# Performance work log

Measured on AMD Instinct MI355X. Metric: run time of the kernel, lower is better.

Reference implementation:

```python
import jax, jax.numpy as jnp
import numpy as np

B, I, H = 16384, 1024, 1024
W_SCALE = 0.03  # keep gate pre-activations in a sane range (mimics small init)


def setup_inputs() -> dict:
    key = jax.random.key(0)
    ks = jax.random.split(key, 7)
    return {
        "x": jax.random.normal(ks[0], (B, I), dtype=jnp.float32),
        "c": jax.random.normal(ks[1], (B, H), dtype=jnp.float32),
        "h": jax.random.normal(ks[2], (B, H), dtype=jnp.float32),
        # gate order along axis 0: f (forget), i (input), k (cell cand), o (output)
        "Wx": jax.random.normal(ks[3], (4, H, I), dtype=jnp.float32) * W_SCALE,
        "bx": jax.random.normal(ks[4], (4, H), dtype=jnp.float32) * W_SCALE,
        "Wh": jax.random.normal(ks[5], (4, H, H), dtype=jnp.float32) * W_SCALE,
        "bh": jax.random.normal(ks[6], (4, H), dtype=jnp.float32) * W_SCALE,
    }


def reference(x, c, h, Wx, bx, Wh, bh):
    # Fused equivalent of the 8 tiny nn.Linear calls: one stacked GEMM each
    # for input->hidden and hidden->hidden. pre: [B, 4, H]
    pre = (jnp.einsum('bi,ghi->bgh', x, Wx)
           + jnp.einsum('bk,ghk->bgh', h, Wh)
           + bx[None] + bh[None])
    f = jax.nn.sigmoid(pre[:, 0])   # forget gate (w1/r1)
    i = jax.nn.sigmoid(pre[:, 1])   # input gate  (w2/r2)
    k = jnp.tanh(pre[:, 2])         # cell candidate (w3/r3)
    o = jax.nn.sigmoid(pre[:, 3])   # output gate (w4/r4)
    c_new = f * c + i * k
    h_new = o * jnp.tanh(c_new)
    return (o, c_new, h_new)
```

## Files before the change

kernel.cpp:

```cpp
#include <hip/hip_runtime.h>
#include <hip/hip_bf16.h>
#include <cstdint>

#define DI __device__ __forceinline__

typedef __attribute__((ext_vector_type(4))) float f32x4;
typedef __attribute__((ext_vector_type(8))) short bf16x8;

static constexpr int B_ = 16384, I_ = 1024, H_ = 1024;
static constexpr int M = B_;
static constexpr int N = 4 * H_;
static constexpr int K = I_ + H_;
static constexpr int NT = K / 64;

static constexpr size_t OFF_A  = 0;
static constexpr size_t OFF_W  = OFF_A + (size_t)M * K * 2;
static constexpr size_t OFF_BI = OFF_W + (size_t)N * K * 2;

DI unsigned short f2bf(float f) {
    union { float f; unsigned u; } v; v.f = f;
    unsigned r = v.u + 0x7FFFu + ((v.u >> 16) & 1u);
    return (unsigned short)(r >> 16);
}

__global__ void cvt_kernel(const float* __restrict__ x, const float* __restrict__ h,
                           const float* __restrict__ Wx, const float* __restrict__ Wh,
                           unsigned short* __restrict__ A, unsigned short* __restrict__ W)
{
    long tid = (long)blockIdx.x * blockDim.x + threadIdx.x;
    long row = tid >> 9;
    int  col = (int)(tid & 511) * 4;
    const float* src;
    unsigned short* dst;
    if (row < M) {
        src = (col < I_) ? x + (size_t)row * I_ + col
                         : h + (size_t)row * H_ + (col - I_);
        dst = A + (size_t)row * K + col;
    } else {
        int r = (int)(row - M);
        int gate = (r >> 4) & 3;
        int hcol = ((r >> 6) << 4) | (r & 15);
        int srow = gate * H_ + hcol;
        src = (col < I_) ? Wx + (size_t)srow * I_ + col
                         : Wh + (size_t)srow * H_ + (col - I_);
        dst = W + (size_t)r * K + col;
    }
    float4 v = *(const float4*)src;
    ushort4 o;
    o.x = f2bf(v.x); o.y = f2bf(v.y); o.z = f2bf(v.z); o.w = f2bf(v.w);
    *(ushort4*)dst = o;
}

__global__ void bias_kernel(const float* __restrict__ bx, const float* __restrict__ bh,
                            float* __restrict__ bias)
{
    int r = blockIdx.x * blockDim.x + threadIdx.x;
    if (r < N) {
        int gate = (r >> 4) & 3;
        int hcol = ((r >> 6) << 4) | (r & 15);
        int s = gate * H_ + hcol;
        bias[r] = bx[s] + bh[s];
    }
}

DI void stage_half(const unsigned short* __restrict__ g, int grow0, int kcol,
                   unsigned short* ldsbase, int tid)
{
    const int w    = tid >> 6, lane = tid & 63;
    const int rsub = (w << 3) + (lane >> 3);
    const int kk   = kcol + (((lane & 7) ^ (lane >> 3)) << 3);
#pragma unroll
    for (int l = 0; l < 2; ++l) {
        const unsigned short* gp = g + (size_t)(grow0 + (l << 6) + rsub) * K + kk;
        unsigned short* lp = ldsbase + (((l << 6) + (w << 3)) << 6);
        __builtin_amdgcn_global_load_lds(
            (const __attribute__((address_space(1))) void*)gp,
            (__attribute__((address_space(3))) void*)lp, 16, 0, 0);
    }
}

DI bf16x8 ldfrag(const unsigned short* tile, int row, int ks, int lane)
{
    const int sl = ((ks << 2) + (lane >> 4)) ^ (lane & 7);
    return *(const bf16x8*)(tile + (row << 6) + (sl << 3));
}

DI float sigf(float v) { return 1.f / (1.f + __expf(-v)); }
DI float tanhfast(float v) {
    float vc = fminf(fmaxf(v, -15.f), 15.f);
    float e  = __expf(2.f * vc);
    return (e - 1.f) / (e + 1.f);
}

__global__ __launch_bounds__(512, 2) void gemm_lstm(
    const unsigned short* __restrict__ Abf, const unsigned short* __restrict__ Wbf,
    const float* __restrict__ bias, const float* __restrict__ c,
    float* __restrict__ out)
{
    __shared__ __align__(16) unsigned short sh[65536];

    const int tid  = threadIdx.x;
    const int lane = tid & 63;
    const int wid  = tid >> 6;
    const int wr   = wid >> 2;
    const int wc   = wid & 3;

    const int bid  = blockIdx.x;
    const int xcd  = bid & 7;
    const int loc  = bid >> 3;
    const int nbk  = (xcd << 1) | (loc & 1);
    const int mbk  = loc >> 1;
    const int brow = mbk << 8, bcol = nbk << 8;

    const int l15  = lane & 15;
    const int rA0  = (wr << 7) + l15;
    const int rB0  = (wc << 6) + l15;

    f32x4 acc[8][4];
#pragma unroll
    for (int i = 0; i < 8; ++i)
#pragma unroll
        for (int j = 0; j < 4; ++j) acc[i][j] = f32x4{0.f, 0.f, 0.f, 0.f};
    bf16x8 a[4][2], b[4][2];

    {
        stage_half(Abf, brow,       0, sh,         tid);
        stage_half(Abf, brow + 128, 0, sh + 8192,  tid);
        stage_half(Wbf, bcol,       0, sh + 16384, tid);
        stage_half(Wbf, bcol + 128, 0, sh + 24576, tid);
        asm volatile("s_waitcnt vmcnt(0)" ::: "memory");
        __builtin_amdgcn_s_barrier();
    }

    for (int t = 0; t < NT; ++t) {
        const int q = t & 1;
        unsigned short* curA = sh + q * 32768;
        unsigned short* curB = curA + 16384;
        unsigned short* nxtA = sh + (q ^ 1) * 32768;
        unsigned short* nxtB = nxtA + 16384;
        const int k1 = ((t + 1) & 31) << 6;

        stage_half(Abf, brow,       k1, nxtA,        tid);
        stage_half(Abf, brow + 128, k1, nxtA + 8192, tid);
        stage_half(Wbf, bcol,       k1, nxtB,        tid);
        stage_half(Wbf, bcol + 128, k1, nxtB + 8192, tid);

#pragma unroll
        for (int n = 0; n < 4; ++n)
#pragma unroll
            for (int ks = 0; ks < 2; ++ks)
                b[n][ks] = ldfrag(curB, rB0 + n * 16, ks, lane);
#pragma unroll
        for (int m = 0; m < 4; ++m)
#pragma unroll
            for (int ks = 0; ks < 2; ++ks)
                a[m][ks] = ldfrag(curA, rA0 + m * 16, ks, lane);

#pragma unroll
        for (int ks = 0; ks < 2; ++ks)
#pragma unroll
            for (int m = 0; m < 4; ++m)
#pragma unroll
                for (int n = 0; n < 4; ++n)
                    acc[m][n] = __builtin_amdgcn_mfma_f32_16x16x32_bf16(
                        a[m][ks], b[n][ks], acc[m][n], 0, 0, 0);

#pragma unroll
        for (int m = 0; m < 4; ++m)
#pragma unroll
            for (int ks = 0; ks < 2; ++ks)
                a[m][ks] = ldfrag(curA, rA0 + 64 + m * 16, ks, lane);

#pragma unroll
        for (int ks = 0; ks < 2; ++ks)
#pragma unroll
            for (int m = 0; m < 4; ++m)
#pragma unroll
                for (int n = 0; n < 4; ++n)
                    acc[4 + m][n] = __builtin_amdgcn_mfma_f32_16x16x32_bf16(
                        a[m][ks], b[n][ks], acc[4 + m][n], 0, 0, 0);

        asm volatile("s_waitcnt vmcnt(0)" ::: "memory");
        __builtin_amdgcn_s_barrier();
    }

    const int hcol  = (((nbk << 2) + wc) << 4) + l15;
    const int crow0 = brow + (wr << 7) + ((lane >> 4) << 2);
    const int cb0   = bcol + (wc << 6) + l15;
    const float bs0 = bias[cb0];
    const float bs1 = bias[cb0 + 16];
    const float bs2 = bias[cb0 + 32];
    const float bs3 = bias[cb0 + 48];
    const size_t P  = (size_t)B_ * H_;
#pragma unroll
    for (int mf = 0; mf < 8; ++mf) {
#pragma unroll
        for (int j = 0; j < 4; ++j) {
            const int row = crow0 + mf * 16 + j;
            const size_t base = (size_t)row * H_ + hcol;
            float fg = sigf(acc[mf][0][j] + bs0);
            float ig = sigf(acc[mf][1][j] + bs1);
            float kg = tanhfast(acc[mf][2][j] + bs2);
            float og = sigf(acc[mf][3][j] + bs3);
            float cv = c[base];
            float cn = fg * cv + ig * kg;
            float hn = og * tanhfast(cn);
            out[base]         = og;
            out[P + base]     = cn;
            out[2 * P + base] = hn;
        }
    }
}

extern "C" void kernel_launch(void* const* d_in, const int* in_sizes, int n_in,
                              void* d_out, int out_size, void* d_ws, size_t ws_size,
                              hipStream_t stream)
{
    const float* x  = (const float*)d_in[0];
    const float* c  = (const float*)d_in[1];
    const float* h  = (const float*)d_in[2];
    const float* Wx = (const float*)d_in[3];
    const float* bx = (const float*)d_in[4];
    const float* Wh = (const float*)d_in[5];
    const float* bh = (const float*)d_in[6];

    unsigned short* Abf  = (unsigned short*)((char*)d_ws + OFF_A);
    unsigned short* Wbf  = (unsigned short*)((char*)d_ws + OFF_W);
    float*          bias = (float*)((char*)d_ws + OFF_BI);
    float*          out  = (float*)d_out;

    cvt_kernel<<<40960, 256, 0, stream>>>(x, h, Wx, Wh, Abf, Wbf);
    bias_kernel<<<16, 256, 0, stream>>>(bx, bh, bias);
    gemm_lstm<<<(M / 256) * (N / 256), 512, 0, stream>>>(
        Abf, Wbf, bias, c, out);
}
```

Measured before the change: 330.1 us.

## Shrink GEMM tile to 128x256 with K-step 32 for higher occupancy

```diff
diff --git a/kernel.cpp b/kernel.cpp
--- a/kernel.cpp
+++ b/kernel.cpp
@@ -11,7 +11,7 @@
 static constexpr int M = B_;
 static constexpr int N = 4 * H_;
 static constexpr int K = I_ + H_;
-static constexpr int NT = K / 64;
+static constexpr int NS = K / 32;
 
 static constexpr size_t OFF_A  = 0;
 static constexpr size_t OFF_W  = OFF_A + (size_t)M * K * 2;
@@ -63,26 +63,23 @@
     }
 }
 
-DI void stage_half(const unsigned short* __restrict__ g, int grow0, int kcol,
-                   unsigned short* ldsbase, int tid)
+DI void stage_A(const unsigned short* __restrict__ g, int grow0, int kcol,
+                unsigned short* ldsbase, int tid)
 {
     const int w    = tid >> 6, lane = tid & 63;
-    const int rsub = (w << 3) + (lane >> 3);
-    const int kk   = kcol + (((lane & 7) ^ (lane >> 3)) << 3);
-#pragma unroll
-    for (int l = 0; l < 2; ++l) {
-        const unsigned short* gp = g + (size_t)(grow0 + (l << 6) + rsub) * K + kk;
-        unsigned short* lp = ldsbase + (((l << 6) + (w << 3)) << 6);
-        __builtin_amdgcn_global_load_lds(
-            (const __attribute__((address_space(1))) void*)gp,
-            (__attribute__((address_space(3))) void*)lp, 16, 0, 0);
-    }
-}
-
-DI bf16x8 ldfrag(const unsigned short* tile, int row, int ks, int lane)
-{
-    const int sl = ((ks << 2) + (lane >> 4)) ^ (lane & 7);
-    return *(const bf16x8*)(tile + (row << 6) + (sl << 3));
+    const int row  = grow0 + (w << 4) + (lane >> 2);
+    const int kk   = kcol + ((((lane & 3) - ((lane >> 3) & 3)) & 3) << 3);
+    const unsigned short* gp = g + (size_t)row * K + kk;
+    unsigned short* lp = ldsbase + (w << 9);
+    __builtin_amdgcn_global_load_lds(
+        (const __attribute__((address_space(1))) void*)gp,
+        (__attribute__((address_space(3))) void*)lp, 16, 0, 0);
+}
+
+DI bf16x8 ldfrag(const unsigned short* tile, int row, int lane)
+{
+    const int sl = ((lane >> 4) + (row >> 1)) & 3;
+    return *(const bf16x8*)(tile + (row << 5) + (sl << 3));
 }
 
 DI float sigf(float v) { return 1.f / (1.f + __expf(-v)); }
@@ -92,12 +89,12 @@
     return (e - 1.f) / (e + 1.f);
 }
 
-__global__ __launch_bounds__(512, 2) void gemm_lstm(
+__global__ __launch_bounds__(512, 4) void gemm_lstm(
     const unsigned short* __restrict__ Abf, const unsigned short* __restrict__ Wbf,
     const float* __restrict__ bias, const float* __restrict__ c,
     float* __restrict__ out)
 {
-    __shared__ __align__(16) unsigned short sh[65536];
+    __shared__ __align__(16) unsigned short sh[24576];
 
     const int tid  = threadIdx.x;
     const int lane = tid & 63;
@@ -110,82 +107,57 @@
     const int loc  = bid >> 3;
     const int nbk  = (xcd << 1) | (loc & 1);
     const int mbk  = loc >> 1;
-    const int brow = mbk << 8, bcol = nbk << 8;
+    const int brow = mbk << 7, bcol = nbk << 8;
 
     const int l15  = lane & 15;
-    const int rA0  = (wr << 7) + l15;
+    const int rA0  = (wr << 6) + l15;
     const int rB0  = (wc << 6) + l15;
 
-    f32x4 acc[8][4];
-#pragma unroll
-    for (int i = 0; i < 8; ++i)
+    f32x4 acc[4][4];
+#pragma unroll
+    for (int i = 0; i < 4; ++i)
 #pragma unroll
         for (int j = 0; j < 4; ++j) acc[i][j] = f32x4{0.f, 0.f, 0.f, 0.f};
-    bf16x8 a[4][2], b[4][2];
+    bf16x8 a[4], b[4];
 
     {
-        stage_half(Abf, brow,       0, sh,         tid);
-        stage_half(Abf, brow + 128, 0, sh + 8192,  tid);
-        stage_half(Wbf, bcol,       0, sh + 16384, tid);
-        stage_half(Wbf, bcol + 128, 0, sh + 24576, tid);
+        stage_A(Abf, brow,       0, sh,         tid);
+        stage_A(Wbf, bcol,       0, sh + 8192,  tid);
+        stage_A(Wbf, bcol + 128, 0, sh + 12288, tid);
         asm volatile("s_waitcnt vmcnt(0)" ::: "memory");
         __builtin_amdgcn_s_barrier();
     }
 
-    for (int t = 0; t < NT; ++t) {
+    for (int t = 0; t < NS; ++t) {
         const int q = t & 1;
-        unsigned short* curA = sh + q * 32768;
-        unsigned short* curB = curA + 16384;
-        unsigned short* nxtA = sh + (q ^ 1) * 32768;
-        unsigned short* nxtB = nxtA + 16384;
-        const int k1 = ((t + 1) & 31) << 6;
-
-        stage_half(Abf, brow,       k1, nxtA,        tid);
-        stage_half(Abf, brow + 128, k1, nxtA + 8192, tid);
-        stage_half(Wbf, bcol,       k1, nxtB,        tid);
-        stage_half(Wbf, bcol + 128, k1, nxtB + 8192, tid);
-
-#pragma unroll
-        for (int n = 0; n < 4; ++n)
-#pragma unroll
-            for (int ks = 0; ks < 2; ++ks)
-                b[n][ks] = ldfrag(curB, rB0 + n * 16, ks, lane);
+        unsigned short* curA = sh + (q << 12);
+        unsigned short* curB = sh + 8192 + (q << 13);
+        unsigned short* nxtA = sh + ((q ^ 1) << 12);
+        unsigned short* nxtB = sh + 8192 + ((q ^ 1) << 13);
+        const int k1 = ((t + 1) & 63) << 5;
+
+        stage_A(Abf, brow,       k1, nxtA,        tid);
+        stage_A(Wbf, bcol,       k1, nxtB,        tid);
+        stage_A(Wbf, bcol + 128, k1, nxtB + 4096, tid);
+
+#pragma unroll
+        for (int m = 0; m < 4; ++m) a[m] = ldfrag(curA, rA0 + m * 16, lane);
+#pragma unroll
+        for (int n = 0; n < 4; ++n) b[n] = ldfrag(curB, rB0 + n * 16, lane);
+
 #pragma unroll
         for (int m = 0; m < 4; ++m)
 #pragma unroll
-            for (int ks = 0; ks < 2; ++ks)
-                a[m][ks] = ldfrag(curA, rA0 + m * 16, ks, lane);
-
-#pragma unroll
-        for (int ks = 0; ks < 2; ++ks)
-#pragma unroll
-            for (int m = 0; m < 4; ++m)
-#pragma unroll
-                for (int n = 0; n < 4; ++n)
-                    acc[m][n] = __builtin_amdgcn_mfma_f32_16x16x32_bf16(
-                        a[m][ks], b[n][ks], acc[m][n], 0, 0, 0);
-
-#pragma unroll
-        for (int m = 0; m < 4; ++m)
-#pragma unroll
-            for (int ks = 0; ks < 2; ++ks)
-                a[m][ks] = ldfrag(curA, rA0 + 64 + m * 16, ks, lane);
-
-#pragma unroll
-        for (int ks = 0; ks < 2; ++ks)
-#pragma unroll
-            for (int m = 0; m < 4; ++m)
-#pragma unroll
-                for (int n = 0; n < 4; ++n)
-                    acc[4 + m][n] = __builtin_amdgcn_mfma_f32_16x16x32_bf16(
-                        a[m][ks], b[n][ks], acc[4 + m][n], 0, 0, 0);
+            for (int n = 0; n < 4; ++n)
+                acc[m][n] = __builtin_amdgcn_mfma_f32_16x16x32_bf16(
+                    a[m], b[n], acc[m][n], 0, 0, 0);
 
         asm volatile("s_waitcnt vmcnt(0)" ::: "memory");
         __builtin_amdgcn_s_barrier();
     }
 
     const int hcol  = (((nbk << 2) + wc) << 4) + l15;
-    const int crow0 = brow + (wr << 7) + ((lane >> 4) << 2);
+    const int crow0 = brow + (wr << 6) + ((lane >> 4) << 2);
     const int cb0   = bcol + (wc << 6) + l15;
     const float bs0 = bias[cb0];
     const float bs1 = bias[cb0 + 16];
@@ -193,7 +165,7 @@
     const float bs3 = bias[cb0 + 48];
     const size_t P  = (size_t)B_ * H_;
 #pragma unroll
-    for (int mf = 0; mf < 8; ++mf) {
+    for (int mf = 0; mf < 4; ++mf) {
 #pragma unroll
         for (int j = 0; j < 4; ++j) {
             const int row = crow0 + mf * 16 + j;
@@ -231,6 +203,6 @@
 
     cvt_kernel<<<40960, 256, 0, stream>>>(x, h, Wx, Wh, Abf, Wbf);
     bias_kernel<<<16, 256, 0, stream>>>(bx, bh, bias);
-    gemm_lstm<<<(M / 256) * (N / 256), 512, 0, stream>>>(
+    gemm_lstm<<<(M / 128) * (N / 256), 512, 0, stream>>>(
         Abf, Wbf, bias, c, out);
 }
```

After: 358.4 us. +8.6%, slower.

## Switch GEMM to 32x32x16 MFMA with 64x128 warp tiles and regrouped gates

Applied to the files above, without the earlier changes.

```diff
diff --git a/kernel.cpp b/kernel.cpp
--- a/kernel.cpp
+++ b/kernel.cpp
@@ -4,8 +4,9 @@
 
 #define DI __device__ __forceinline__
 
-typedef __attribute__((ext_vector_type(4))) float f32x4;
-typedef __attribute__((ext_vector_type(8))) short bf16x8;
+typedef __attribute__((ext_vector_type(4)))  float f32x4;
+typedef __attribute__((ext_vector_type(16))) float f32x16;
+typedef __attribute__((ext_vector_type(8)))  short bf16x8;
 
 static constexpr int B_ = 16384, I_ = 1024, H_ = 1024;
 static constexpr int M = B_;
@@ -38,8 +39,8 @@
         dst = A + (size_t)row * K + col;
     } else {
         int r = (int)(row - M);
-        int gate = (r >> 4) & 3;
-        int hcol = ((r >> 6) << 4) | (r & 15);
+        int gate = (r >> 5) & 3;
+        int hcol = ((r >> 7) << 5) | (r & 31);
         int srow = gate * H_ + hcol;
         src = (col < I_) ? Wx + (size_t)srow * I_ + col
                          : Wh + (size_t)srow * H_ + (col - I_);
@@ -56,8 +57,8 @@
 {
     int r = blockIdx.x * blockDim.x + threadIdx.x;
     if (r < N) {
-        int gate = (r >> 4) & 3;
-        int hcol = ((r >> 6) << 4) | (r & 15);
+        int gate = (r >> 5) & 3;
+        int hcol = ((r >> 7) << 5) | (r & 31);
         int s = gate * H_ + hcol;
         bias[r] = bx[s] + bh[s];
     }
@@ -79,9 +80,9 @@
     }
 }
 
-DI bf16x8 ldfrag(const unsigned short* tile, int row, int ks, int lane)
-{
-    const int sl = ((ks << 2) + (lane >> 4)) ^ (lane & 7);
+DI bf16x8 ldfrag32(const unsigned short* tile, int row, int s16, int lane)
+{
+    const int sl = (((s16 << 1) + (lane >> 5)) ^ (row & 7));
     return *(const bf16x8*)(tile + (row << 6) + (sl << 3));
 }
 
@@ -102,8 +103,8 @@
     const int tid  = threadIdx.x;
     const int lane = tid & 63;
     const int wid  = tid >> 6;
-    const int wr   = wid >> 2;
-    const int wc   = wid & 3;
+    const int wr   = wid >> 1;
+    const int wc   = wid & 1;
 
     const int bid  = blockIdx.x;
     const int xcd  = bid & 7;
@@ -112,16 +113,18 @@
     const int mbk  = loc >> 1;
     const int brow = mbk << 8, bcol = nbk << 8;
 
-    const int l15  = lane & 15;
-    const int rA0  = (wr << 7) + l15;
-    const int rB0  = (wc << 6) + l15;
-
-    f32x4 acc[8][4];
-#pragma unroll
-    for (int i = 0; i < 8; ++i)
-#pragma unroll
-        for (int j = 0; j < 4; ++j) acc[i][j] = f32x4{0.f, 0.f, 0.f, 0.f};
-    bf16x8 a[4][2], b[4][2];
+    const int l31  = lane & 31;
+    const int rA0  = (wr << 6) + l31;
+    const int rB0  = (wc << 7) + l31;
+
+    f32x16 acc[2][4];
+#pragma unroll
+    for (int i = 0; i < 2; ++i)
+#pragma unroll
+        for (int j = 0; j < 4; ++j)
+#pragma unroll
+            for (int e = 0; e < 16; ++e) acc[i][j][e] = 0.f;
+    bf16x8 a[4], b[4][4];
 
     {
         stage_half(Abf, brow,       0, sh,         tid);
@@ -146,62 +149,51 @@
         stage_half(Wbf, bcol + 128, k1, nxtB + 8192, tid);
 
 #pragma unroll
-        for (int n = 0; n < 4; ++n)
-#pragma unroll
-            for (int ks = 0; ks < 2; ++ks)
-                b[n][ks] = ldfrag(curB, rB0 + n * 16, ks, lane);
-#pragma unroll
-        for (int m = 0; m < 4; ++m)
-#pragma unroll
-            for (int ks = 0; ks < 2; ++ks)
-                a[m][ks] = ldfrag(curA, rA0 + m * 16, ks, lane);
-
-#pragma unroll
-        for (int ks = 0; ks < 2; ++ks)
-#pragma unroll
-            for (int m = 0; m < 4; ++m)
-#pragma unroll
-                for (int n = 0; n < 4; ++n)
-                    acc[m][n] = __builtin_amdgcn_mfma_f32_16x16x32_bf16(
-                        a[m][ks], b[n][ks], acc[m][n], 0, 0, 0);
-
-#pragma unroll
-        for (int m = 0; m < 4; ++m)
-#pragma unroll
-            for (int ks = 0; ks < 2; ++ks)
-                a[m][ks] = ldfrag(curA, rA0 + 64 + m * 16, ks, lane);
-
-#pragma unroll
-        for (int ks = 0; ks < 2; ++ks)
-#pragma unroll
-            for (int m = 0; m < 4; ++m)
-#pragma unroll
-                for (int n = 0; n < 4; ++n)
-                    acc[4 + m][n] = __builtin_amdgcn_mfma_f32_16x16x32_bf16(
-                        a[m][ks], b[n][ks], acc[4 + m][n], 0, 0, 0);
+        for (int nt = 0; nt < 4; ++nt)
+#pragma unroll
+            for (int s = 0; s < 4; ++s)
+                b[nt][s] = ldfrag32(curB, rB0 + nt * 32, s, lane);
+
+#pragma unroll
+        for (int s = 0; s < 4; ++s) a[s] = ldfrag32(curA, rA0, s, lane);
+#pragma unroll
+        for (int s = 0; s < 4; ++s)
+#pragma unroll
+            for (int nt = 0; nt < 4; ++nt)
+                acc[0][nt] = __builtin_amdgcn_mfma_f32_32x32x16_bf16(
+                    a[s], b[nt][s], acc[0][nt], 0, 0, 0);
+
+#pragma unroll
+        for (int s = 0; s < 4; ++s) a[s] = ldfrag32(curA, rA0 + 32, s, lane);
+#pragma unroll
+        for (int s = 0; s < 4; ++s)
+#pragma unroll
+            for (int nt = 0; nt < 4; ++nt)
+                acc[1][nt] = __builtin_amdgcn_mfma_f32_32x32x16_bf16(
+                    a[s], b[nt][s], acc[1][nt], 0, 0, 0);
 
         asm volatile("s_waitcnt vmcnt(0)" ::: "memory");
         __builtin_amdgcn_s_barrier();
     }
 
-    const int hcol  = (((nbk << 2) + wc) << 4) + l15;
-    const int crow0 = brow + (wr << 7) + ((lane >> 4) << 2);
-    const int cb0   = bcol + (wc << 6) + l15;
-    const float bs0 = bias[cb0];
-    const float bs1 = bias[cb0 + 16];
-    const float bs2 = bias[cb0 + 32];
-    const float bs3 = bias[cb0 + 48];
+    const int c0    = bcol + (wc << 7);
+    const int hcol  = ((c0 >> 7) << 5) + l31;
+    const float bs0 = bias[c0 +       l31];
+    const float bs1 = bias[c0 +  32 + l31];
+    const float bs2 = bias[c0 +  64 + l31];
+    const float bs3 = bias[c0 +  96 + l31];
+    const int rbase = brow + (wr << 6) + ((lane >> 5) << 2);
     const size_t P  = (size_t)B_ * H_;
 #pragma unroll
-    for (int mf = 0; mf < 8; ++mf) {
-#pragma unroll
-        for (int j = 0; j < 4; ++j) {
-            const int row = crow0 + mf * 16 + j;
+    for (int mt = 0; mt < 2; ++mt) {
+#pragma unroll
+        for (int r = 0; r < 16; ++r) {
+            const int row = rbase + mt * 32 + (r & 3) + ((r >> 2) << 3);
             const size_t base = (size_t)row * H_ + hcol;
-            float fg = sigf(acc[mf][0][j] + bs0);
-            float ig = sigf(acc[mf][1][j] + bs1);
-            float kg = tanhfast(acc[mf][2][j] + bs2);
-            float og = sigf(acc[mf][3][j] + bs3);
+            float fg = sigf(acc[mt][0][r] + bs0);
+            float ig = sigf(acc[mt][1][r] + bs1);
+            float kg = tanhfast(acc[mt][2][r] + bs2);
+            float og = sigf(acc[mt][3][r] + bs3);
             float cv = c[base];
             float cn = fg * cv + ig * kg;
             float hn = og * tanhfast(cn);
```

Result: slower. 350.6 us (+6.2%).
